# Performance work log

Hardware: AMD Instinct MI355X
Metric: run time of the kernel (lower is better)

Reference implementation:

```python
import jax, jax.numpy as jnp
import numpy as np

TEMP_LEN = 16
TARGET_LEN = 22
NUM_HEADS = 16
DIM = 512
B = 16
N = TEMP_LEN**2 + TARGET_LEN**2  # 740


def bias_index(w_len, h_len):
    # Swin-style relative position index, matches torch getBiasIndex
    coords = jnp.stack(jnp.meshgrid(jnp.arange(h_len), jnp.arange(w_len), indexing='ij'))  # [2,h,w]
    flat = coords.reshape(2, -1)                       # [2, L]
    rel = flat[:, :, None] - flat[:, None, :]          # [2, L, L]
    rel = rel.transpose(1, 2, 0)                       # [L, L, 2]
    r0 = (rel[..., 0] + w_len - 1) * (2 * w_len - 1)
    r1 = rel[..., 1] + h_len - 1
    return r0 + r1                                     # [L, L] int32


def setup_inputs() -> dict:
    key = jax.random.key(0)
    ks = jax.random.split(key, 12)
    C, H = DIM, NUM_HEADS
    s = 0.0002
    return {
        'x': jax.random.normal(ks[0], (B, N, C), jnp.float32),
        'W_qkv': jax.random.normal(ks[1], (C, 3 * C), jnp.float32) * (1.0 / np.sqrt(C)),
        'b_qkv': jnp.zeros((3 * C,), jnp.float32),
        'W_proj': jax.random.normal(ks[2], (C, C), jnp.float32) * (1.0 / np.sqrt(C)),
        'b_proj': jnp.zeros((C,), jnp.float32),
        'bias_table_target': jax.random.normal(ks[3], ((2 * TARGET_LEN - 1) ** 2, H), jnp.float32) * s,
        'bias_table_temp': jax.random.normal(ks[4], ((2 * TEMP_LEN - 1) ** 2, H), jnp.float32) * s,
        'temp_target_table': jax.random.normal(ks[5], (H, TARGET_LEN**2, 1), jnp.float32) * s,
        'target_temp_table': jax.random.normal(ks[6], (H, TEMP_LEN**2, 1), jnp.float32) * s,
        'temp_target_line': jax.random.normal(ks[7], (H, 1, TEMP_LEN**2), jnp.float32) * s,
        'target_temp_line': jax.random.normal(ks[8], (H, 1, TARGET_LEN**2), jnp.float32) * s,
    }


def reference(x, W_qkv, b_qkv, W_proj, b_proj,
              bias_table_target, bias_table_temp,
              temp_target_table, target_temp_table,
              temp_target_line, target_temp_line):
    Bb, Nn, C = x.shape
    H = NUM_HEADS
    hd = C // H
    scale = hd ** -0.5

    qkv = (x @ W_qkv + b_qkv).reshape(Bb, Nn, 3, H, hd).transpose(2, 0, 3, 1, 4)
    q, k, v = qkv[0], qkv[1], qkv[2]  # each [B, H, N, hd]

    # --- relative position bias, concat of 4 blocks -> [H, N, N] ---
    idx_temp = bias_index(TEMP_LEN, TEMP_LEN)        # [256, 256]
    idx_target = bias_index(TARGET_LEN, TARGET_LEN)  # [484, 484]
    temp_bias = bias_table_temp[idx_temp].transpose(2, 0, 1)      # [H, 256, 256]
    target_bias = bias_table_target[idx_target].transpose(2, 0, 1)  # [H, 484, 484]
    temp_target = temp_target_table + temp_target_line            # [H, 484, 256]
    target_temp = target_temp_table + target_temp_line            # [H, 256, 484]
    left = jnp.concatenate([temp_bias, temp_target], axis=1)      # [H, 740, 256]
    right = jnp.concatenate([target_temp, target_bias], axis=1)   # [H, 740, 484]
    bias = jnp.concatenate([left, right], axis=2)                 # [H, 740, 740]

    attn = jnp.einsum('bhqd,bhkd->bhqk', q, k) * scale + bias[None]
    attn = jax.nn.softmax(attn, axis=-1)
    out = jnp.einsum('bhqk,bhkd->bhqd', attn, v)                  # [B, H, N, hd]
    out = out.transpose(0, 2, 1, 3).reshape(Bb, Nn, C)
    return out @ W_proj + b_proj
```

## Files before the change

kernel.cpp:

```cpp
#include <hip/hip_runtime.h>
#include <hip/hip_bf16.h>
#include <hip/hip_fp16.h>
#include <stdint.h>
#include <stddef.h>

typedef __attribute__((ext_vector_type(8))) short short8;
typedef __attribute__((ext_vector_type(4))) float f32x4;
typedef unsigned short ushort_t;

#define NHEADS 16
#define HD 32
#define NQ 740
#define NB 16
#define MROWS (NB*NQ)
#define CD 512
#define KDIM 512
#define VSTRIDE 768
#define NQT 48
#define PTS 40
#define QS2 0.2550400865f
#define LOG2E 1.4426950409f
#define NEG_BIG -43000.0f

static __device__ __forceinline__ void gld_lds16(const void* g, void* l) {
    __builtin_amdgcn_global_load_lds((const __attribute__((address_space(1))) void*)g,
                                     (__attribute__((address_space(3))) void*)l,
                                     16, 0, 0);
}

static __device__ __forceinline__ float ldf(const void* p, int i, int fl) {
    return fl ? ((const float*)p)[i] : (float)((const __hip_bfloat16*)p)[i];
}
static __device__ __forceinline__ ushort_t f2bf(float f) {
    __hip_bfloat16 h(f);
    return *reinterpret_cast<ushort_t*>(&h);
}
static __device__ __forceinline__ float fexp2(float x) {
#if __has_builtin(__builtin_amdgcn_exp2f)
    return __builtin_amdgcn_exp2f(x);
#else
    return exp2f(x);
#endif
}
static __device__ __forceinline__ unsigned int f2e5(float f) {
    __half h = __float2half(f);
    unsigned short hb = *reinterpret_cast<unsigned short*>(&h);
    return (((unsigned int)hb + 0x7fu + ((hb >> 8) & 1u)) >> 8) & 0xffu;
}
static __device__ __forceinline__ f32x4 bias4f8(unsigned int b) {
    f32x4 c;
    #pragma unroll
    for (int i = 0; i < 4; ++i) {
        union { unsigned short u; __half h; } cv;
        cv.u = (unsigned short)(((b >> (8 * i)) & 0xffu) << 8);
        c[i] = __half2float(cv.h);
    }
    return c;
}
static __device__ __forceinline__ void pkstore(__hip_bfloat16* dst, f32x4 c) {
    __hip_bfloat162* d = (__hip_bfloat162*)dst;
    d[0] = __float22bfloat162_rn(make_float2(c[0], c[1]));
    d[1] = __float22bfloat162_rn(make_float2(c[2], c[3]));
}
static __device__ __forceinline__ uint2 pk4(float a, float b, float c, float d) {
    __hip_bfloat162 p01 = __float22bfloat162_rn(make_float2(a, b));
    __hip_bfloat162 p23 = __float22bfloat162_rn(make_float2(c, d));
    uint2 u;
    u.x = *reinterpret_cast<unsigned int*>(&p01);
    u.y = *reinterpret_cast<unsigned int*>(&p23);
    return u;
}

__global__ __launch_bounds__(64) void sniff_k(const unsigned int* __restrict__ w,
                                              int* __restrict__ flag) {
    int cnt = 0;
    for (int i = threadIdx.x; i < 1024; i += 64) {
        unsigned int e = (w[i] >> 7) & 0xFFu;
        cnt += (e > 135u) ? 1 : 0;
    }
    #pragma unroll
    for (int d = 1; d < 64; d <<= 1) cnt += __shfl_xor(cnt, d);
    if (threadIdx.x == 0) *flag = (cnt > 16) ? 1 : 0;
}

__global__ __launch_bounds__(256) void convx_k(const void* __restrict__ src,
                                               ushort4* __restrict__ dst,
                                               int nquads, const int* __restrict__ flag) {
    int i = blockIdx.x * 256 + threadIdx.x;
    if (i >= nquads) return;
    if (*flag) {
        float4 v = ((const float4*)src)[i];
        ushort4 o;
        o.x = f2bf(v.x); o.y = f2bf(v.y); o.z = f2bf(v.z); o.w = f2bf(v.w);
        dst[i] = o;
    } else {
        dst[i] = ((const ushort4*)src)[i];
    }
}

__global__ __launch_bounds__(256) void transpose_k(const void* __restrict__ src,
                                                   __hip_bfloat16* __restrict__ dst,
                                                   int R, int C, const int* __restrict__ flag) {
    __shared__ __hip_bfloat16 tile[32][33];
    const int fl = *flag;
    int bx = blockIdx.x * 32;
    int by = blockIdx.y * 32;
    int tx = threadIdx.x;
    for (int r = threadIdx.y; r < 32; r += 8)
        tile[r][tx] = __hip_bfloat16(ldf(src, (by + r) * C + bx + tx, fl));
    __syncthreads();
    for (int r = threadIdx.y; r < 32; r += 8)
        dst[(size_t)(bx + r) * R + by + tx] = tile[tx][r];
}

__global__ __launch_bounds__(256) void biasF_k(
    const void* __restrict__ btT,
    const void* __restrict__ btt,
    const void* __restrict__ ttab,
    const void* __restrict__ tgtab,
    const void* __restrict__ ttln,
    const void* __restrict__ tgln,
    unsigned int* __restrict__ biasF, const int* __restrict__ flag) {
    const int fl = *flag;
    const int blk = blockIdx.x;
    const int hh = blk / NQT;
    const int qt = blk - hh * NQT;
    for (int idx = threadIdx.x; idx < 48 * 64; idx += 256) {
        const int kb = idx >> 6;
        const int lane = idx & 63;
        const int lr = lane & 15, kc = lane >> 4;
        int i = qt * 16 + lr; if (i > NQ - 1) i = NQ - 1;
        unsigned int pk = 0;
        #pragma unroll
        for (int r = 0; r < 4; ++r) {
            int c = kb * 16 + kc * 4 + r;
            float v;
            if (c >= NQ) {
                v = NEG_BIG;
            } else if (i < 256) {
                if (c < 256) {
                    int t = ((i >> 4) - (c >> 4) + 15) * 31 + ((i & 15) - (c & 15) + 15);
                    v = ldf(btt, t * 16 + hh, fl) * LOG2E;
                } else {
                    v = (ldf(tgtab, hh * 256 + i, fl) + ldf(tgln, hh * 484 + (c - 256), fl)) * LOG2E;
                }
            } else {
                int ii = i - 256;
                if (c < 256) {
                    v = (ldf(ttab, hh * 484 + ii, fl) + ldf(ttln, hh * 256 + c, fl)) * LOG2E;
                } else {
                    int jj = c - 256;
                    int a = ii / 22, b2 = ii - a * 22;
                    int a2 = jj / 22, b3 = jj - a2 * 22;
                    int t = (a - a2 + 21) * 43 + (b2 - b3 + 21);
                    v = ldf(btT, t * 16 + hh, fl) * LOG2E;
                }
            }
            pk |= f2e5(v) << (8 * r);
        }
        biasF[(size_t)blk * 48 * 64 + idx] = pk;
    }
}

__global__ __launch_bounds__(256) void gemm_qkv(
    const __hip_bfloat16* __restrict__ A,
    const __hip_bfloat16* __restrict__ Bt,
    const void* __restrict__ biasv,
    __hip_bfloat16* __restrict__ Qw,
    __hip_bfloat16* __restrict__ Kw,
    __hip_bfloat16* __restrict__ Vtw,
    const int* __restrict__ flag) {
    __shared__ __attribute__((aligned(16))) short sStage[3 * 12288];
    const int tid = threadIdx.x;
    const int lane = tid & 63;
    const int wv = tid >> 6;
    const int lr = lane & 15, kc = lane >> 4;
    const int m0 = blockIdx.y * 256;
    const int n0 = blockIdx.x * 128;
    const int fl = *flag;
    const int M = MROWS;

    auto stage = [&](int s) {
        char* bb = (char*)sStage + (s % 3) * 24576;
        const int k0 = s * 32;
        #pragma unroll
        for (int it = 0; it < 6; ++it) {
            int idx = it * 256 + tid;
            if (idx < 1024) {
                int r = idx >> 2, c = idx & 3;
                int gr = m0 + r; if (gr > M - 1) gr = M - 1;
                gld_lds16(A + (size_t)gr * KDIM + k0 + c * 8, bb + idx * 16);
            } else {
                int u = idx - 1024;
                int r = u >> 2, c = u & 3;
                gld_lds16(Bt + (size_t)(n0 + r) * KDIM + k0 + c * 8, bb + 16384 + u * 16);
            }
        }
    };

    f32x4 acc[4][8] = {};
    stage(0);
    stage(1);

    for (int ks = 0; ks < 16; ++ks) {
        asm volatile("" ::: "memory");
        if (ks < 15) __builtin_amdgcn_s_waitcnt(0x0076);
        else         __builtin_amdgcn_s_waitcnt(0x0070);
        __builtin_amdgcn_s_barrier();
        asm volatile("" ::: "memory");
        if (ks + 2 < 16) stage(ks + 2);

        const char* bb = (const char*)sStage + (ks % 3) * 24576;
        const short* cA = (const short*)bb;
        const short* cB = (const short*)(bb + 16384);
        short8 af[4], bfr[8];
        #pragma unroll
        for (int t = 0; t < 4; ++t)
            af[t] = *(const short8*)&cA[(wv * 64 + t * 16 + lr) * 32 + kc * 8];
        #pragma unroll
        for (int t = 0; t < 8; ++t)
            bfr[t] = *(const short8*)&cB[(t * 16 + lr) * 32 + kc * 8];
        #pragma unroll
        for (int i = 0; i < 4; ++i)
            #pragma unroll
            for (int j = 0; j < 8; ++j)
                acc[i][j] = __builtin_amdgcn_mfma_f32_16x16x32_bf16(af[i], bfr[j], acc[i][j], 0, 0, 0);
    }

    const int s = n0 >> 9;
    short* Tw = (short*)((char*)sStage + 24576) + wv * 2560;
    const int gmr = m0 + wv * 64 + lane;
    int gmrc = gmr < M ? gmr : M - 1;
    int bq = gmrc / NQ;
    int nnq = gmrc - bq * NQ;
    const int gmv = m0 + wv * 64 + (lane & 15) * 4;
    int gmvc = gmv < M ? gmv : M - 1;
    int bv2 = gmvc / NQ;
    int nnv = gmvc - bv2 * NQ;

    #pragma unroll
    for (int t = 0; t < 4; ++t) {
        const int hh = ((n0 >> 5) + t) & 15;
        float bva = ldf(biasv, n0 + t * 32 + lr, fl);
        float bvb = ldf(biasv, n0 + t * 32 + 16 + lr, fl);
        asm volatile("" ::: "memory");
        if (s == 2) {
            #pragma unroll
            for (int i = 0; i < 4; ++i) {
                int nl = i * 16 + kc * 4;
                uint2 ua = pk4(acc[i][2*t][0] + bva, acc[i][2*t][1] + bva,
                               acc[i][2*t][2] + bva, acc[i][2*t][3] + bva);
                uint2 ub = pk4(acc[i][2*t+1][0] + bvb, acc[i][2*t+1][1] + bvb,
                               acc[i][2*t+1][2] + bvb, acc[i][2*t+1][3] + bvb);
                *(uint2*)(void*)&Tw[lr * 72 + nl]        = ua;
                *(uint2*)(void*)&Tw[(16 + lr) * 72 + nl] = ub;
            }
        } else {
            float sc = (s == 0) ? QS2 : 1.0f;
            #pragma unroll
            for (int i = 0; i < 4; ++i)
                #pragma unroll
                for (int r = 0; r < 4; ++r) {
                    int nl = i * 16 + kc * 4 + r;
                    Tw[nl * 40 + lr]      = (short)f2bf((acc[i][2*t][r]   + bva) * sc);
                    Tw[nl * 40 + 16 + lr] = (short)f2bf((acc[i][2*t+1][r] + bvb) * sc);
                }
        }
        asm volatile("" ::: "memory");
        __builtin_amdgcn_s_waitcnt(0xc07f);
        asm volatile("" ::: "memory");
        if (s == 2) {
            if (gmv < M) {
                size_t bh = (size_t)(bv2 * 16 + hh);
                #pragma unroll
                for (int i2 = 0; i2 < 8; ++i2) {
                    int d = (lane >> 4) + i2 * 4;
                    uint2 u = *(const uint2*)(const void*)&Tw[d * 72 + (lane & 15) * 4];
                    *(uint2*)(void*)(Vtw + (bh * HD + d) * VSTRIDE + nnv) = u;
                }
            }
        } else {
            if (gmr < M) {
                size_t bh = (size_t)(bq * 16 + hh);
                __hip_bfloat16* dst = (s == 0 ? Qw : Kw) + (bh * NQ + nnq) * HD;
                #pragma unroll
                for (int c = 0; c < 4; ++c) {
                    short8 u = *(const short8*)(const void*)&Tw[lane * 40 + c * 8];
                    *(short8*)(void*)(dst + c * 8) = u;
                }
            }
        }
        asm volatile("" ::: "memory");
        __builtin_amdgcn_s_waitcnt(0xc07f);
        asm volatile("" ::: "memory");
    }
}

__global__ __launch_bounds__(256) void gemm_bt(
    const __hip_bfloat16* __restrict__ A,
    const __hip_bfloat16* __restrict__ Bt,
    const void* __restrict__ biasv,
    int M,
    __hip_bfloat16* __restrict__ Out,
    float* __restrict__ OutF,
    const int* __restrict__ flag) {
    __shared__ __attribute__((aligned(16))) short sStage[3 * 8192];
    const int tid = threadIdx.x;
    const int lane = tid & 63;
    const int wv = tid >> 6;
    const int wr = wv >> 1, wc = wv & 1;
    const int lr = lane & 15, kc = lane >> 4;
    const int m0 = blockIdx.y * 128;
    const int n0 = blockIdx.x * 128;
    const int fl = *flag;

    auto stage = [&](int s) {
        char* bb = (char*)sStage + (s % 3) * 16384;
        const int k0 = s * 32;
        #pragma unroll
        for (int it = 0; it < 2; ++it) {
            int idx = it * 256 + tid;
            int r = idx >> 2;
            int c = idx & 3;
            int gr = m0 + r; if (gr > M - 1) gr = M - 1;
            gld_lds16(A + (size_t)gr * KDIM + k0 + c * 8, bb + idx * 16);
            gld_lds16(Bt + (size_t)(n0 + r) * KDIM + k0 + c * 8, bb + 8192 + idx * 16);
        }
    };

    f32x4 acc[4][4] = {};
    stage(0);
    stage(1);

    for (int ks = 0; ks < 16; ++ks) {
        asm volatile("" ::: "memory");
        if (ks < 15) __builtin_amdgcn_s_waitcnt(0x0074);
        else         __builtin_amdgcn_s_waitcnt(0x0070);
        __builtin_amdgcn_s_barrier();
        asm volatile("" ::: "memory");
        if (ks + 2 < 16) stage(ks + 2);

        const char* bb = (const char*)sStage + (ks % 3) * 16384;
        const short* cA = (const short*)bb;
        const short* cB = (const short*)(bb + 8192);
        short8 af[4], bfr[4];
        #pragma unroll
        for (int t = 0; t < 4; ++t)
            af[t] = *(const short8*)&cA[(wr * 64 + t * 16 + lr) * 32 + kc * 8];
        #pragma unroll
        for (int t = 0; t < 4; ++t)
            bfr[t] = *(const short8*)&cB[(wc * 64 + t * 16 + lr) * 32 + kc * 8];
        #pragma unroll
        for (int i = 0; i < 4; ++i)
            #pragma unroll
            for (int j = 0; j < 4; ++j)
                acc[i][j] = __builtin_amdgcn_mfma_f32_16x16x32_bf16(af[i], bfr[j], acc[i][j], 0, 0, 0);
    }

    #pragma unroll
    for (int i = 0; i < 4; ++i) {
        #pragma unroll
        for (int j = 0; j < 4; ++j) {
            int gn = n0 + wc * 64 + j * 16 + lr;
            float bv = ldf(biasv, gn, fl);
            #pragma unroll
            for (int r = 0; r < 4; ++r) {
                int gm = m0 + wr * 64 + i * 16 + kc * 4 + r;
                if (gm < M) {
                    float v = acc[i][j][r] + bv;
                    if (fl) OutF[(size_t)gm * CD + gn] = v;
                    else    Out[(size_t)gm * CD + gn] = __hip_bfloat16(v);
                }
            }
        }
    }
}

__global__ __launch_bounds__(256) void attn_k(
    const __hip_bfloat16* __restrict__ Qw,
    const __hip_bfloat16* __restrict__ Kw,
    const __hip_bfloat16* __restrict__ Vtw,
    const unsigned int* __restrict__ biasF,
    __hip_bfloat16* __restrict__ AO) {
    __shared__ __attribute__((aligned(16))) short sStage[3 * 2048];
    __shared__ __attribute__((aligned(16))) __hip_bfloat16 Pt[4][32 * PTS];

    const int tid = threadIdx.x;
    const int wv = tid >> 6;
    const int pair = blockIdx.x * 4 + wv;
    const int bh = blockIdx.y;
    const int hh = bh & 15;
    const int b = bh >> 4;
    const int q0 = pair * 32;
    const int lane = tid & 63;
    const int lr = lane & 15, kc = lane >> 4;

    const __hip_bfloat16* Qb = Qw + (size_t)bh * NQ * HD;
    const __hip_bfloat16* Kb = Kw + (size_t)bh * NQ * HD;
    const __hip_bfloat16* Vb = Vtw + (size_t)bh * HD * VSTRIDE;
    __hip_bfloat16* Pw = &Pt[wv][0];

    short8 qfA = *(const short8*)(const void*)(Qb + (q0 + lr) * HD + kc * 8);
    short8 qfB = *(const short8*)(const void*)(Qb + (q0 + 16 + lr) * HD + kc * 8);

    short8 onesf;
    {
        short s1 = (lr == 0) ? (short)0x3F80 : (short)0;
        #pragma unroll
        for (int j = 0; j < 8; ++j) onesf[j] = s1;
    }

    const unsigned int* bt0 = biasF + (size_t)(hh * NQT + 2 * pair) * 48 * 64 + lane;
    const unsigned int* bt1 = bt0 + 48 * 64;

    unsigned int brA0[2], brA1[2], brB0[2], brB1[2];
    brA0[0] = bt0[0];  brA1[0] = bt0[64];
    brB0[0] = bt1[0];  brB1[0] = bt1[64];

    {
        const void* src;
        if (tid < 128) src = Kb + (tid >> 2) * HD + (tid & 3) * 8;
        else { int u = tid - 128; src = Vb + (u >> 2) * VSTRIDE + (u & 3) * 8; }
        gld_lds16(src, (char*)sStage + tid * 16);
    }
    asm volatile("" ::: "memory");

    f32x4 oa0 = {}, ob0 = {}, ol0 = {};
    f32x4 oa1 = {}, ob1 = {}, ol1 = {};

    #pragma unroll
    for (int ks = 0; ks < 24; ++ks) {
        const int cur = ks & 1, nxt = cur ^ 1;
        if (ks < 23) {
            brA0[nxt] = bt0[(2 * ks + 2) * 64];
            brA1[nxt] = bt0[(2 * ks + 3) * 64];
            brB0[nxt] = bt1[(2 * ks + 2) * 64];
            brB1[nxt] = bt1[(2 * ks + 3) * 64];
            const int k0n = (ks + 1) * 32;
            const int nb = ((ks + 1) % 3) * 4096;
            const void* src;
            if (tid < 128) src = Kb + (k0n + (tid >> 2)) * HD + (tid & 3) * 8;
            else { int u = tid - 128; src = Vb + (u >> 2) * VSTRIDE + k0n + (u & 3) * 8; }
            gld_lds16(src, (char*)sStage + nb + tid * 16);
        }
        asm volatile("" ::: "memory");
        if (ks < 23) __builtin_amdgcn_s_waitcnt(0x0F75);
        else         __builtin_amdgcn_s_waitcnt(0x0F70);
        __builtin_amdgcn_s_barrier();
        asm volatile("" ::: "memory");

        const short* sK = (const short*)((const char*)sStage + (ks % 3) * 4096);
        const short* sV = sK + 1024;
        short8 kf0 = *(const short8*)&sK[lr * 32 + kc * 8];
        short8 kf1 = *(const short8*)&sK[(16 + lr) * 32 + kc * 8];
        short8 vf0 = *(const short8*)&sV[lr * 32 + kc * 8];
        short8 vf1 = *(const short8*)&sV[(16 + lr) * 32 + kc * 8];

        f32x4 c0 = bias4f8(brA0[cur]);
        f32x4 c1 = bias4f8(brA1[cur]);
        f32x4 c2 = bias4f8(brB0[cur]);
        f32x4 c3 = bias4f8(brB1[cur]);

        c0 = __builtin_amdgcn_mfma_f32_16x16x32_bf16(kf0, qfA, c0, 0, 0, 0);
        c1 = __builtin_amdgcn_mfma_f32_16x16x32_bf16(kf1, qfA, c1, 0, 0, 0);
        c2 = __builtin_amdgcn_mfma_f32_16x16x32_bf16(kf0, qfB, c2, 0, 0, 0);
        c3 = __builtin_amdgcn_mfma_f32_16x16x32_bf16(kf1, qfB, c3, 0, 0, 0);

        #pragma unroll
        for (int r = 0; r < 4; ++r) {
            c0[r] = fexp2(c0[r]); c1[r] = fexp2(c1[r]);
            c2[r] = fexp2(c2[r]); c3[r] = fexp2(c3[r]);
        }
        pkstore(Pw + lr * PTS + kc * 4, c0);
        pkstore(Pw + lr * PTS + 16 + kc * 4, c1);
        pkstore(Pw + (16 + lr) * PTS + kc * 4, c2);
        pkstore(Pw + (16 + lr) * PTS + 16 + kc * 4, c3);
        asm volatile("" ::: "memory");
        __builtin_amdgcn_s_waitcnt(0xc07f);
        asm volatile("" ::: "memory");

        short8 pfA = *(const short8*)(const void*)(Pw + lr * PTS + kc * 8);
        short8 pfB = *(const short8*)(const void*)(Pw + (16 + lr) * PTS + kc * 8);

        oa0 = __builtin_amdgcn_mfma_f32_16x16x32_bf16(pfA, vf0, oa0, 0, 0, 0);
        ob0 = __builtin_amdgcn_mfma_f32_16x16x32_bf16(pfA, vf1, ob0, 0, 0, 0);
        ol0 = __builtin_amdgcn_mfma_f32_16x16x32_bf16(pfA, onesf, ol0, 0, 0, 0);
        oa1 = __builtin_amdgcn_mfma_f32_16x16x32_bf16(pfB, vf0, oa1, 0, 0, 0);
        ob1 = __builtin_amdgcn_mfma_f32_16x16x32_bf16(pfB, vf1, ob1, 0, 0, 0);
        ol1 = __builtin_amdgcn_mfma_f32_16x16x32_bf16(pfB, onesf, ol1, 0, 0, 0);
    }

    #pragma unroll
    for (int r = 0; r < 4; ++r) {
        int row = kc * 4 + r;
        float lA = __shfl(ol0[r], lane & 48);
        float lB = __shfl(ol1[r], lane & 48);
        float liA = 1.0f / lA, liB = 1.0f / lB;
        int orA = q0 + row, orB = q0 + 16 + row;
        if (orA < NQ) {
            size_t base = ((size_t)b * NQ + orA) * CD + hh * HD;
            AO[base + lr]      = __hip_bfloat16(oa0[r] * liA);
            AO[base + 16 + lr] = __hip_bfloat16(ob0[r] * liA);
        }
        if (orB < NQ) {
            size_t base = ((size_t)b * NQ + orB) * CD + hh * HD;
            AO[base + lr]      = __hip_bfloat16(oa1[r] * liB);
            AO[base + 16 + lr] = __hip_bfloat16(ob1[r] * liB);
        }
    }
}

extern "C" void kernel_launch(void* const* d_in, const int* in_sizes, int n_in,
                              void* d_out, int out_size, void* d_ws, size_t ws_size,
                              hipStream_t stream) {
    char* ws = (char*)d_ws;
    size_t off = 0;
    auto carve = [&](size_t bytes) {
        char* p = ws + off;
        off += (bytes + 255) & ~(size_t)255;
        return p;
    };
    int* flagp = (int*)carve(256);
    __hip_bfloat16* Qw    = (__hip_bfloat16*)carve((size_t)256 * NQ * HD * 2);
    __hip_bfloat16* Kw    = (__hip_bfloat16*)carve((size_t)256 * NQ * HD * 2);
    __hip_bfloat16* Vtw   = (__hip_bfloat16*)carve((size_t)256 * HD * VSTRIDE * 2);
    __hip_bfloat16* WqT   = (__hip_bfloat16*)carve((size_t)1536 * 512 * 2);
    __hip_bfloat16* WpT   = (__hip_bfloat16*)carve((size_t)512 * 512 * 2);
    unsigned int*   biasF = (unsigned int*)carve((size_t)16 * NQT * 48 * 64 * 4);
    __hip_bfloat16* Xb    = (__hip_bfloat16*)carve((size_t)MROWS * CD * 2);
    __hip_bfloat16* AO    = Xb;
    (void)ws_size; (void)in_sizes; (void)n_in; (void)out_size;

    sniff_k<<<dim3(1), dim3(64), 0, stream>>>((const unsigned int*)d_in[1], flagp);
    convx_k<<<dim3(5920), dim3(256), 0, stream>>>(d_in[0], (ushort4*)Xb, MROWS * CD / 4, flagp);
    transpose_k<<<dim3(48, 16), dim3(32, 8), 0, stream>>>(d_in[1], WqT, 512, 1536, flagp);
    transpose_k<<<dim3(16, 16), dim3(32, 8), 0, stream>>>(d_in[3], WpT, 512, 512, flagp);
    biasF_k<<<dim3(16 * NQT), dim3(256), 0, stream>>>(d_in[5], d_in[6], d_in[7], d_in[8],
                                                      d_in[9], d_in[10], biasF, flagp);
    gemm_qkv<<<dim3(12, 47), dim3(256), 0, stream>>>(Xb, WqT, d_in[2],
        Qw, Kw, Vtw, flagp);
    attn_k<<<dim3(6, 256), dim3(256), 0, stream>>>(Qw, Kw, Vtw, biasF, AO);
    gemm_bt<<<dim3(4, 93), dim3(256), 0, stream>>>(AO, WpT, d_in[4], MROWS,
        (__hip_bfloat16*)d_out, (float*)d_out, flagp);
}
```

Baseline: 225.8 us.

## Fuse prep kernels, use hardware bf8 unpack, and remap K/V LDS staging layout

Merges the x conversion, both weight transposes and the bias-table build into one prep_k launch with block-range dispatch, which cuts launch overhead and the gaps between small kernels. The bias decode in attention now uses the cvt_pk_f32_bf8 builtin when the compiler provides it, in place of scalar half conversions. The K/V staging into LDS is remapped so each 8-element column chunk is stored contiguously, which changes the fragment read pattern and likely reduces LDS bank conflicts. The grid-stride conversion loop now runs over fewer blocks, and the hardware bf8 decode must round exactly like the old manual decode.

```diff
diff --git a/kernel.cpp b/kernel.cpp
--- a/kernel.cpp
+++ b/kernel.cpp
@@ -6,6 +6,7 @@
 
 typedef __attribute__((ext_vector_type(8))) short short8;
 typedef __attribute__((ext_vector_type(4))) float f32x4;
+typedef __attribute__((ext_vector_type(2))) float f32x2;
 typedef unsigned short ushort_t;
 
 #define NHEADS 16
@@ -47,6 +48,15 @@
     unsigned short hb = *reinterpret_cast<unsigned short*>(&h);
     return (((unsigned int)hb + 0x7fu + ((hb >> 8) & 1u)) >> 8) & 0xffu;
 }
+#if __has_builtin(__builtin_amdgcn_cvt_pk_f32_bf8)
+static __device__ __forceinline__ f32x4 bias4f8(unsigned int b) {
+    f32x2 lo = __builtin_amdgcn_cvt_pk_f32_bf8((int)b, false);
+    f32x2 hi = __builtin_amdgcn_cvt_pk_f32_bf8((int)b, true);
+    f32x4 c;
+    c[0] = lo[0]; c[1] = lo[1]; c[2] = hi[0]; c[3] = hi[1];
+    return c;
+}
+#else
 static __device__ __forceinline__ f32x4 bias4f8(unsigned int b) {
     f32x4 c;
     #pragma unroll
@@ -57,6 +67,7 @@
     }
     return c;
 }
+#endif
 static __device__ __forceinline__ void pkstore(__hip_bfloat16* dst, f32x4 c) {
     __hip_bfloat162* d = (__hip_bfloat162*)dst;
     d[0] = __float22bfloat162_rn(make_float2(c[0], c[1]));
@@ -83,51 +94,62 @@
     if (threadIdx.x == 0) *flag = (cnt > 16) ? 1 : 0;
 }
 
-__global__ __launch_bounds__(256) void convx_k(const void* __restrict__ src,
-                                               ushort4* __restrict__ dst,
-                                               int nquads, const int* __restrict__ flag) {
-    int i = blockIdx.x * 256 + threadIdx.x;
-    if (i >= nquads) return;
-    if (*flag) {
-        float4 v = ((const float4*)src)[i];
-        ushort4 o;
-        o.x = f2bf(v.x); o.y = f2bf(v.y); o.z = f2bf(v.z); o.w = f2bf(v.w);
-        dst[i] = o;
-    } else {
-        dst[i] = ((const ushort4*)src)[i];
-    }
-}
-
-__global__ __launch_bounds__(256) void transpose_k(const void* __restrict__ src,
-                                                   __hip_bfloat16* __restrict__ dst,
-                                                   int R, int C, const int* __restrict__ flag) {
+#define PREP_CONV 1480
+#define PREP_TA   768
+#define PREP_TB   256
+#define PREP_BIAS 768
+__global__ __launch_bounds__(256) void prep_k(
+    const void* __restrict__ x, ushort4* __restrict__ Xb,
+    const void* __restrict__ Wqkv, __hip_bfloat16* __restrict__ WqT,
+    const void* __restrict__ Wproj, __hip_bfloat16* __restrict__ WpT,
+    const void* __restrict__ btT, const void* __restrict__ btt,
+    const void* __restrict__ ttab, const void* __restrict__ tgtab,
+    const void* __restrict__ ttln, const void* __restrict__ tgln,
+    unsigned int* __restrict__ biasF,
+    const int* __restrict__ flag) {
     __shared__ __hip_bfloat16 tile[32][33];
+    const int bid = blockIdx.x;
+    const int tid = threadIdx.x;
     const int fl = *flag;
-    int bx = blockIdx.x * 32;
-    int by = blockIdx.y * 32;
-    int tx = threadIdx.x;
-    for (int r = threadIdx.y; r < 32; r += 8)
-        tile[r][tx] = __hip_bfloat16(ldf(src, (by + r) * C + bx + tx, fl));
-    __syncthreads();
-    for (int r = threadIdx.y; r < 32; r += 8)
-        dst[(size_t)(bx + r) * R + by + tx] = tile[tx][r];
-}
-
-__global__ __launch_bounds__(256) void biasF_k(
-    const void* __restrict__ btT,
-    const void* __restrict__ btt,
-    const void* __restrict__ ttab,
-    const void* __restrict__ tgtab,
-    const void* __restrict__ ttln,
-    const void* __restrict__ tgln,
-    unsigned int* __restrict__ biasF, const int* __restrict__ flag) {
-    const int fl = *flag;
-    const int blk = blockIdx.x;
+
+    if (bid < PREP_CONV) {
+        const int n = MROWS * CD / 4;
+        for (int i = bid * 256 + tid; i < n; i += PREP_CONV * 256) {
+            if (fl) {
+                float4 v = ((const float4*)x)[i];
+                ushort4 o;
+                o.x = f2bf(v.x); o.y = f2bf(v.y); o.z = f2bf(v.z); o.w = f2bf(v.w);
+                Xb[i] = o;
+            } else {
+                Xb[i] = ((const ushort4*)x)[i];
+            }
+        }
+        return;
+    }
+    if (bid < PREP_CONV + PREP_TA + PREP_TB) {
+        const void* src; __hip_bfloat16* dst; int R, C, lb;
+        if (bid < PREP_CONV + PREP_TA) {
+            src = Wqkv; dst = WqT; R = 512; C = 1536; lb = bid - PREP_CONV;
+        } else {
+            src = Wproj; dst = WpT; R = 512; C = 512; lb = bid - PREP_CONV - PREP_TA;
+        }
+        int nbx = C / 32;
+        int bx = (lb % nbx) * 32;
+        int by = (lb / nbx) * 32;
+        int tx = tid & 31, ty = tid >> 5;
+        for (int r = ty; r < 32; r += 8)
+            tile[r][tx] = __hip_bfloat16(ldf(src, (by + r) * C + bx + tx, fl));
+        __syncthreads();
+        for (int r = ty; r < 32; r += 8)
+            dst[(size_t)(bx + r) * R + by + tx] = tile[tx][r];
+        return;
+    }
+    const int blk = bid - (PREP_CONV + PREP_TA + PREP_TB);
     const int hh = blk / NQT;
     const int qt = blk - hh * NQT;
-    for (int idx = threadIdx.x; idx < 48 * 64; idx += 256) {
+    for (int idx = tid; idx < 48 * 64; idx += 256) {
+        const int lane = idx & 63;
         const int kb = idx >> 6;
-        const int lane = idx & 63;
         const int lr = lane & 15, kc = lane >> 4;
         int i = qt * 16 + lr; if (i > NQ - 1) i = NQ - 1;
         unsigned int pk = 0;
@@ -419,8 +441,8 @@
 
     {
         const void* src;
-        if (tid < 128) src = Kb + (tid >> 2) * HD + (tid & 3) * 8;
-        else { int u = tid - 128; src = Vb + (u >> 2) * VSTRIDE + (u & 3) * 8; }
+        if (tid < 128) src = Kb + (tid & 31) * HD + (tid >> 5) * 8;
+        else { int u = tid - 128; src = Vb + (u & 31) * VSTRIDE + ((u >> 5) & 3) * 8; }
         gld_lds16(src, (char*)sStage + tid * 16);
     }
     asm volatile("" ::: "memory");
@@ -439,8 +461,8 @@
             const int k0n = (ks + 1) * 32;
             const int nb = ((ks + 1) % 3) * 4096;
             const void* src;
-            if (tid < 128) src = Kb + (k0n + (tid >> 2)) * HD + (tid & 3) * 8;
-            else { int u = tid - 128; src = Vb + (u >> 2) * VSTRIDE + k0n + (u & 3) * 8; }
+            if (tid < 128) src = Kb + (k0n + (tid & 31)) * HD + (tid >> 5) * 8;
+            else { int u = tid - 128; src = Vb + (u & 31) * VSTRIDE + k0n + ((u >> 5) & 3) * 8; }
             gld_lds16(src, (char*)sStage + nb + tid * 16);
         }
         asm volatile("" ::: "memory");
@@ -451,10 +473,10 @@
 
         const short* sK = (const short*)((const char*)sStage + (ks % 3) * 4096);
         const short* sV = sK + 1024;
-        short8 kf0 = *(const short8*)&sK[lr * 32 + kc * 8];
-        short8 kf1 = *(const short8*)&sK[(16 + lr) * 32 + kc * 8];
-        short8 vf0 = *(const short8*)&sV[lr * 32 + kc * 8];
-        short8 vf1 = *(const short8*)&sV[(16 + lr) * 32 + kc * 8];
+        short8 kf0 = *(const short8*)&sK[kc * 256 + lr * 8];
+        short8 kf1 = *(const short8*)&sK[kc * 256 + (16 + lr) * 8];
+        short8 vf0 = *(const short8*)&sV[kc * 256 + lr * 8];
+        short8 vf1 = *(const short8*)&sV[kc * 256 + (16 + lr) * 8];
 
         f32x4 c0 = bias4f8(brA0[cur]);
         f32x4 c1 = bias4f8(brA1[cur]);
@@ -532,11 +554,9 @@
     (void)ws_size; (void)in_sizes; (void)n_in; (void)out_size;
 
     sniff_k<<<dim3(1), dim3(64), 0, stream>>>((const unsigned int*)d_in[1], flagp);
-    convx_k<<<dim3(5920), dim3(256), 0, stream>>>(d_in[0], (ushort4*)Xb, MROWS * CD / 4, flagp);
-    transpose_k<<<dim3(48, 16), dim3(32, 8), 0, stream>>>(d_in[1], WqT, 512, 1536, flagp);
-    transpose_k<<<dim3(16, 16), dim3(32, 8), 0, stream>>>(d_in[3], WpT, 512, 512, flagp);
-    biasF_k<<<dim3(16 * NQT), dim3(256), 0, stream>>>(d_in[5], d_in[6], d_in[7], d_in[8],
-                                                      d_in[9], d_in[10], biasF, flagp);
+    prep_k<<<dim3(PREP_CONV + PREP_TA + PREP_TB + PREP_BIAS), dim3(256), 0, stream>>>(
+        d_in[0], (ushort4*)Xb, d_in[1], WqT, d_in[3], WpT,
+        d_in[5], d_in[6], d_in[7], d_in[8], d_in[9], d_in[10], biasF, flagp);
     gemm_qkv<<<dim3(12, 47), dim3(256), 0, stream>>>(Xb, WqT, d_in[2],
         Qw, Kw, Vtw, flagp);
     attn_k<<<dim3(6, 256), dim3(256), 0, stream>>>(Qw, Kw, Vtw, biasF, AO);
```

New measurement: 222.0 us. About the same (-1.7%).
